# Kernel tuning notes

Measured on AMD Instinct MI355X. Metric: run time of the kernel, lower is better.

The kernel has to match this reference:

```python
import jax, jax.numpy as jnp
import numpy as np


def setup_inputs() -> dict:
    key = jax.random.key(0)
    k_x, k_rbf, k_nb, k_w1, k_w2 = jax.random.split(key, 5)
    N, NB, F_DIM, RBF_DIM = 20000, 32, 128, 64
    x = jax.random.normal(k_x, (N, F_DIM), dtype=jnp.float32)
    rbf = jax.random.uniform(k_rbf, (N, NB, RBF_DIM), dtype=jnp.float32)
    neighbors = jax.random.randint(k_nb, (N, NB), 0, N, dtype=jnp.int64)
    # filter network params (Linear(rbf_dim->f_dim), Softplus, Linear(f_dim->f_dim))
    w1 = jax.random.normal(k_w1, (RBF_DIM, F_DIM), dtype=jnp.float32) / np.sqrt(RBF_DIM)
    b1 = jnp.zeros((F_DIM,), dtype=jnp.float32)
    w2 = jax.random.normal(k_w2, (F_DIM, F_DIM), dtype=jnp.float32) / np.sqrt(F_DIM)
    b2 = jnp.zeros((F_DIM,), dtype=jnp.float32)
    return {"x": x, "rbf": rbf, "neighbors": neighbors,
            "w1": w1, "b1": b1, "w2": w2, "b2": b2}


def reference(x, rbf, neighbors, w1, b1, w2, b2):
    # filter network: Linear -> Softplus -> Linear, applied per (atom, neighbor)
    h = jax.nn.softplus(jnp.einsum('anr,rf->anf', rbf, w1) + b1)  # [N, NB, F]
    W = jnp.einsum('ang,gf->anf', h, w2) + b2                      # [N, NB, F]
    x_j = x[neighbors]                                             # gather [N, NB, F]
    return jnp.sum(x_j * W, axis=1)                                # [N, F]
```

## Files before the change

kernel.cpp:

```cpp
#include <hip/hip_runtime.h>
#include <math.h>


#define NATOMS 20000
#define NB     32
#define FD     128
#define RD     64
#define WAVES  8
#define NTILES 2500
#define HSTR   136

typedef short  short8  __attribute__((ext_vector_type(8)));
typedef float  floatx4 __attribute__((ext_vector_type(4)));
typedef float  floatx2 __attribute__((ext_vector_type(2)));

static __device__ __forceinline__ short f2bf(float f) {
  unsigned u = __builtin_bit_cast(unsigned, f);
  u = (u + 0x7FFFu + ((u >> 16) & 1u)) >> 16;
  return (short)u;
}

static __device__ __forceinline__ float softplus(float v) {
  return fmaxf(v, 0.0f) + __logf(1.0f + __expf(-fabsf(v)));
}

__global__ __launch_bounds__(512)
void cfconv_kernel(const float* __restrict__ x,
                   const float* __restrict__ rbf,
                   const int*   __restrict__ nbr,
                   const float* __restrict__ w1,
                   const float* __restrict__ b1,
                   const float* __restrict__ w2,
                   const float* __restrict__ b2,
                   float* __restrict__ out) {
  __shared__ __align__(16) short w1f[16][64][8];
  __shared__ __align__(16) short w2f[32][64][8];
  __shared__ __align__(16) short hbuf[WAVES * 32][HSTR];

  const int tid  = threadIdx.x;
  const int lane = tid & 63;
  const int wv   = tid >> 6;
  const int q    = lane >> 4;
  const int ln   = lane & 15;

  for (int i = tid; i < RD * FD; i += 512) {
    int k = i >> 7, n = i & 127, kk = k & 31;
    w1f[(k >> 5) * 8 + (n >> 4)][(kk >> 3) * 16 + (n & 15)][kk & 7] = f2bf(w1[i]);
  }
  for (int i = tid; i < FD * FD; i += 512) {
    int k = i >> 7, n = i & 127, kk = k & 31;
    w2f[(k >> 5) * 8 + (n >> 4)][(kk >> 3) * 16 + (n & 15)][kk & 7] = f2bf(w2[i]);
  }
  float b1v[8], b2v[8];
#pragma unroll
  for (int nt = 0; nt < 8; ++nt) {
    b1v[nt] = b1[nt * 16 + ln];
    b2v[nt] = b2[nt * 16 + ln];
  }
  __syncthreads();

  for (int tile = blockIdx.x; tile < NTILES; tile += gridDim.x) {
    const int atom = tile * WAVES + wv;
    const int prow = atom * NB;
    const int hrow = wv * 32;

    short8 afrag[2][2];
#pragma unroll
    for (int mt = 0; mt < 2; ++mt) {
      const float* src = rbf + (prow + mt * 16 + ln) * RD + q * 8;
#pragma unroll
      for (int kt = 0; kt < 2; ++kt) {
        floatx4 lo = *(const floatx4*)(src + kt * 32);
        floatx4 hi = *(const floatx4*)(src + kt * 32 + 4);
        short8 f;
        f[0] = f2bf(lo[0]); f[1] = f2bf(lo[1]); f[2] = f2bf(lo[2]); f[3] = f2bf(lo[3]);
        f[4] = f2bf(hi[0]); f[5] = f2bf(hi[1]); f[6] = f2bf(hi[2]); f[7] = f2bf(hi[3]);
        afrag[mt][kt] = f;
      }
    }

    floatx4 acc1[2][8];
#pragma unroll
    for (int mt = 0; mt < 2; ++mt)
#pragma unroll
      for (int nt = 0; nt < 8; ++nt)
        acc1[mt][nt] = floatx4{0.f, 0.f, 0.f, 0.f};
#pragma unroll
    for (int kt = 0; kt < 2; ++kt)
#pragma unroll
      for (int nt = 0; nt < 8; ++nt) {
        short8 bfrag = *(const short8*)&w1f[kt * 8 + nt][lane][0];
#pragma unroll
        for (int mt = 0; mt < 2; ++mt)
          acc1[mt][nt] = __builtin_amdgcn_mfma_f32_16x16x32_bf16(
              afrag[mt][kt], bfrag, acc1[mt][nt], 0, 0, 0);
      }

#pragma unroll
    for (int mt = 0; mt < 2; ++mt)
#pragma unroll
      for (int nt = 0; nt < 8; ++nt)
#pragma unroll
        for (int r = 0; r < 4; ++r)
          hbuf[hrow + mt * 16 + q * 4 + r][nt * 16 + ln] =
              f2bf(softplus(acc1[mt][nt][r] + b1v[nt]));

    short8 hfrag[2][4];
#pragma unroll
    for (int mt = 0; mt < 2; ++mt)
#pragma unroll
      for (int kt = 0; kt < 4; ++kt)
        hfrag[mt][kt] = *(const short8*)&hbuf[hrow + mt * 16 + ln][kt * 32 + q * 8];

    floatx4 acc2[2][8];
#pragma unroll
    for (int mt = 0; mt < 2; ++mt)
#pragma unroll
      for (int nt = 0; nt < 8; ++nt)
        acc2[mt][nt] = floatx4{0.f, 0.f, 0.f, 0.f};
#pragma unroll
    for (int kt = 0; kt < 4; ++kt)
#pragma unroll
      for (int nt = 0; nt < 8; ++nt) {
        short8 bfrag = *(const short8*)&w2f[kt * 8 + nt][lane][0];
#pragma unroll
        for (int mt = 0; mt < 2; ++mt)
          acc2[mt][nt] = __builtin_amdgcn_mfma_f32_16x16x32_bf16(
              hfrag[mt][kt], bfrag, acc2[mt][nt], 0, 0, 0);
      }

#pragma unroll
    for (int mt = 0; mt < 2; ++mt)
#pragma unroll
      for (int nt = 0; nt < 8; ++nt)
#pragma unroll
        for (int r = 0; r < 4; ++r)
          hbuf[hrow + mt * 16 + q * 4 + r][nt * 16 + ln] =
              f2bf(acc2[mt][nt][r] + b2v[nt]);

    const int* nbp = nbr + atom * NB;
    float o0 = 0.f, o1 = 0.f;
#pragma unroll 8
    for (int r = 0; r < NB; ++r) {
      int j = nbp[r];
      floatx2 xv = *(const floatx2*)(x + j * FD + lane * 2);
      unsigned pw = *(const unsigned*)&hbuf[hrow + r][lane * 2];
      o0 += xv[0] * __builtin_bit_cast(float, pw << 16);
      o1 += xv[1] * __builtin_bit_cast(float, pw & 0xFFFF0000u);
    }
    *(floatx2*)(out + atom * FD + lane * 2) = floatx2{o0, o1};
  }
}

extern "C" void kernel_launch(void* const* d_in, const int* in_sizes, int n_in,
                              void* d_out, int out_size, void* d_ws, size_t ws_size,
                              hipStream_t stream) {
  const float* x   = (const float*)d_in[0];
  const float* rbf = (const float*)d_in[1];
  const int*   nbr = (const int*)d_in[2];
  const float* w1  = (const float*)d_in[3];
  const float* b1  = (const float*)d_in[4];
  const float* w2  = (const float*)d_in[5];
  const float* b2  = (const float*)d_in[6];
  float* out = (float*)d_out;

  cfconv_kernel<<<dim3(256), dim3(512), 0, stream>>>(x, rbf, nbr, w1, b1, w2, b2, out);
}
```

Baseline: 310.1 us.

## Fuse second GEMM output directly into neighbor gather, shrink LDS band with XOR swizzle

```diff
diff --git a/kernel.cpp b/kernel.cpp
--- a/kernel.cpp
+++ b/kernel.cpp
@@ -1,30 +1,29 @@
 #include <hip/hip_runtime.h>
+#include <hip/hip_bf16.h>
 #include <math.h>
 
 
-#define NATOMS 20000
 #define NB     32
 #define FD     128
 #define RD     64
 #define WAVES  8
 #define NTILES 2500
-#define HSTR   136
 
 typedef short  short8  __attribute__((ext_vector_type(8)));
 typedef float  floatx4 __attribute__((ext_vector_type(4)));
-typedef float  floatx2 __attribute__((ext_vector_type(2)));
 
-static __device__ __forceinline__ short f2bf(float f) {
-  unsigned u = __builtin_bit_cast(unsigned, f);
-  u = (u + 0x7FFFu + ((u >> 16) & 1u)) >> 16;
-  return (short)u;
+static __device__ __forceinline__ unsigned pk2(float a, float b) {
+  __hip_bfloat162 h = __float22bfloat162_rn(float2{a, b});
+  unsigned u;
+  __builtin_memcpy(&u, &h, sizeof(u));
+  return u;
 }
 
 static __device__ __forceinline__ float softplus(float v) {
   return fmaxf(v, 0.0f) + __logf(1.0f + __expf(-fabsf(v)));
 }
 
-__global__ __launch_bounds__(512)
+__global__ __launch_bounds__(512, 4)
 void cfconv_kernel(const float* __restrict__ x,
                    const float* __restrict__ rbf,
                    const int*   __restrict__ nbr,
@@ -35,7 +34,7 @@
                    float* __restrict__ out) {
   __shared__ __align__(16) short w1f[16][64][8];
   __shared__ __align__(16) short w2f[32][64][8];
-  __shared__ __align__(16) short hbuf[WAVES * 32][HSTR];
+  __shared__ __align__(16) short hbuf[WAVES * 16][128];
 
   const int tid  = threadIdx.x;
   const int lane = tid & 63;
@@ -45,11 +44,11 @@
 
   for (int i = tid; i < RD * FD; i += 512) {
     int k = i >> 7, n = i & 127, kk = k & 31;
-    w1f[(k >> 5) * 8 + (n >> 4)][(kk >> 3) * 16 + (n & 15)][kk & 7] = f2bf(w1[i]);
+    w1f[(k >> 5) * 8 + (n >> 4)][(kk >> 3) * 16 + (n & 15)][kk & 7] = (short)pk2(w1[i], 0.f);
   }
   for (int i = tid; i < FD * FD; i += 512) {
     int k = i >> 7, n = i & 127, kk = k & 31;
-    w2f[(k >> 5) * 8 + (n >> 4)][(kk >> 3) * 16 + (n & 15)][kk & 7] = f2bf(w2[i]);
+    w2f[(k >> 5) * 8 + (n >> 4)][(kk >> 3) * 16 + (n & 15)][kk & 7] = (short)pk2(w2[i], 0.f);
   }
   float b1v[8], b2v[8];
 #pragma unroll
@@ -59,96 +58,107 @@
   }
   __syncthreads();
 
+  short (*band)[128] = &hbuf[wv * 16];
+
   for (int tile = blockIdx.x; tile < NTILES; tile += gridDim.x) {
     const int atom = tile * WAVES + wv;
     const int prow = atom * NB;
-    const int hrow = wv * 32;
 
-    short8 afrag[2][2];
+    floatx4 raw[2][2][2];
 #pragma unroll
     for (int mt = 0; mt < 2; ++mt) {
       const float* src = rbf + (prow + mt * 16 + ln) * RD + q * 8;
 #pragma unroll
       for (int kt = 0; kt < 2; ++kt) {
-        floatx4 lo = *(const floatx4*)(src + kt * 32);
-        floatx4 hi = *(const floatx4*)(src + kt * 32 + 4);
-        short8 f;
-        f[0] = f2bf(lo[0]); f[1] = f2bf(lo[1]); f[2] = f2bf(lo[2]); f[3] = f2bf(lo[3]);
-        f[4] = f2bf(hi[0]); f[5] = f2bf(hi[1]); f[6] = f2bf(hi[2]); f[7] = f2bf(hi[3]);
-        afrag[mt][kt] = f;
+        raw[mt][kt][0] = *(const floatx4*)(src + kt * 32);
+        raw[mt][kt][1] = *(const floatx4*)(src + kt * 32 + 4);
+      }
+    }
+    short8 afrag[2][2];
+#pragma unroll
+    for (int mt = 0; mt < 2; ++mt)
+#pragma unroll
+      for (int kt = 0; kt < 2; ++kt) {
+        union { short8 s8; unsigned u[4]; } f;
+        f.u[0] = pk2(raw[mt][kt][0][0], raw[mt][kt][0][1]);
+        f.u[1] = pk2(raw[mt][kt][0][2], raw[mt][kt][0][3]);
+        f.u[2] = pk2(raw[mt][kt][1][0], raw[mt][kt][1][1]);
+        f.u[3] = pk2(raw[mt][kt][1][2], raw[mt][kt][1][3]);
+        afrag[mt][kt] = f.s8;
+      }
+
+    const int* nbp = nbr + prow;
+    float psum[8];
+#pragma unroll
+    for (int nt = 0; nt < 8; ++nt) psum[nt] = 0.f;
+
+#pragma unroll
+    for (int mt = 0; mt < 2; ++mt) {
+      floatx4 acc1[8];
+#pragma unroll
+      for (int nt = 0; nt < 8; ++nt) acc1[nt] = floatx4{0.f, 0.f, 0.f, 0.f};
+#pragma unroll
+      for (int kt = 0; kt < 2; ++kt)
+#pragma unroll
+        for (int nt = 0; nt < 8; ++nt) {
+          short8 bfrag = *(const short8*)&w1f[kt * 8 + nt][lane][0];
+          acc1[nt] = __builtin_amdgcn_mfma_f32_16x16x32_bf16(
+              afrag[mt][kt], bfrag, acc1[nt], 0, 0, 0);
+        }
+
+#pragma unroll
+      for (int nt = 0; nt < 8; ++nt) {
+        const int c  = nt * 16 + ln;
+        const int cb = c >> 3, cl = c & 7;
+        float s0 = softplus(acc1[nt][0] + b1v[nt]);
+        float s1 = softplus(acc1[nt][1] + b1v[nt]);
+        float s2 = softplus(acc1[nt][2] + b1v[nt]);
+        float s3 = softplus(acc1[nt][3] + b1v[nt]);
+        unsigned u01 = pk2(s0, s1), u23 = pk2(s2, s3);
+        band[q * 4 + 0][(((cb ^ (q * 4 + 0)) & 15) << 3) | cl] = (short)u01;
+        band[q * 4 + 1][(((cb ^ (q * 4 + 1)) & 15) << 3) | cl] = (short)(u01 >> 16);
+        band[q * 4 + 2][(((cb ^ (q * 4 + 2)) & 15) << 3) | cl] = (short)u23;
+        band[q * 4 + 3][(((cb ^ (q * 4 + 3)) & 15) << 3) | cl] = (short)(u23 >> 16);
+      }
+
+      short8 hfrag[4];
+#pragma unroll
+      for (int kt = 0; kt < 4; ++kt) {
+        const int pb = ((kt * 4 + q) ^ ln) & 15;
+        hfrag[kt] = *(const short8*)&band[ln][pb << 3];
+      }
+
+      floatx4 acc2[8];
+#pragma unroll
+      for (int nt = 0; nt < 8; ++nt) acc2[nt] = floatx4{0.f, 0.f, 0.f, 0.f};
+#pragma unroll
+      for (int kt = 0; kt < 4; ++kt)
+#pragma unroll
+        for (int nt = 0; nt < 8; ++nt) {
+          short8 bfrag = *(const short8*)&w2f[kt * 8 + nt][lane][0];
+          acc2[nt] = __builtin_amdgcn_mfma_f32_16x16x32_bf16(
+              hfrag[kt], bfrag, acc2[nt], 0, 0, 0);
+        }
+
+#pragma unroll
+      for (int r = 0; r < 4; ++r) {
+        const int j = nbp[mt * 16 + q * 4 + r];
+        const float* xr = x + j * FD + ln;
+#pragma unroll
+        for (int nt = 0; nt < 8; ++nt)
+          psum[nt] = fmaf(xr[nt * 16], acc2[nt][r] + b2v[nt], psum[nt]);
       }
     }
 
-    floatx4 acc1[2][8];
 #pragma unroll
-    for (int mt = 0; mt < 2; ++mt)
-#pragma unroll
-      for (int nt = 0; nt < 8; ++nt)
-        acc1[mt][nt] = floatx4{0.f, 0.f, 0.f, 0.f};
-#pragma unroll
-    for (int kt = 0; kt < 2; ++kt)
-#pragma unroll
-      for (int nt = 0; nt < 8; ++nt) {
-        short8 bfrag = *(const short8*)&w1f[kt * 8 + nt][lane][0];
-#pragma unroll
-        for (int mt = 0; mt < 2; ++mt)
-          acc1[mt][nt] = __builtin_amdgcn_mfma_f32_16x16x32_bf16(
-              afrag[mt][kt], bfrag, acc1[mt][nt], 0, 0, 0);
-      }
-
-#pragma unroll
-    for (int mt = 0; mt < 2; ++mt)
-#pragma unroll
-      for (int nt = 0; nt < 8; ++nt)
-#pragma unroll
-        for (int r = 0; r < 4; ++r)
-          hbuf[hrow + mt * 16 + q * 4 + r][nt * 16 + ln] =
-              f2bf(softplus(acc1[mt][nt][r] + b1v[nt]));
-
-    short8 hfrag[2][4];
-#pragma unroll
-    for (int mt = 0; mt < 2; ++mt)
-#pragma unroll
-      for (int kt = 0; kt < 4; ++kt)
-        hfrag[mt][kt] = *(const short8*)&hbuf[hrow + mt * 16 + ln][kt * 32 + q * 8];
-
-    floatx4 acc2[2][8];
-#pragma unroll
-    for (int mt = 0; mt < 2; ++mt)
-#pragma unroll
-      for (int nt = 0; nt < 8; ++nt)
-        acc2[mt][nt] = floatx4{0.f, 0.f, 0.f, 0.f};
-#pragma unroll
-    for (int kt = 0; kt < 4; ++kt)
-#pragma unroll
-      for (int nt = 0; nt < 8; ++nt) {
-        short8 bfrag = *(const short8*)&w2f[kt * 8 + nt][lane][0];
-#pragma unroll
-        for (int mt = 0; mt < 2; ++mt)
-          acc2[mt][nt] = __builtin_amdgcn_mfma_f32_16x16x32_bf16(
-              hfrag[mt][kt], bfrag, acc2[mt][nt], 0, 0, 0);
-      }
-
-#pragma unroll
-    for (int mt = 0; mt < 2; ++mt)
-#pragma unroll
-      for (int nt = 0; nt < 8; ++nt)
-#pragma unroll
-        for (int r = 0; r < 4; ++r)
-          hbuf[hrow + mt * 16 + q * 4 + r][nt * 16 + ln] =
-              f2bf(acc2[mt][nt][r] + b2v[nt]);
-
-    const int* nbp = nbr + atom * NB;
-    float o0 = 0.f, o1 = 0.f;
-#pragma unroll 8
-    for (int r = 0; r < NB; ++r) {
-      int j = nbp[r];
-      floatx2 xv = *(const floatx2*)(x + j * FD + lane * 2);
-      unsigned pw = *(const unsigned*)&hbuf[hrow + r][lane * 2];
-      o0 += xv[0] * __builtin_bit_cast(float, pw << 16);
-      o1 += xv[1] * __builtin_bit_cast(float, pw & 0xFFFF0000u);
+    for (int nt = 0; nt < 8; ++nt) {
+      psum[nt] += __shfl_xor(psum[nt], 16);
+      psum[nt] += __shfl_xor(psum[nt], 32);
     }
-    *(floatx2*)(out + atom * FD + lane * 2) = floatx2{o0, o1};
+    float v0 = (q == 0) ? psum[0] : (q == 1) ? psum[2] : (q == 2) ? psum[4] : psum[6];
+    float v1 = (q == 0) ? psum[1] : (q == 1) ? psum[3] : (q == 2) ? psum[5] : psum[7];
+    out[atom * FD + q * 32 + ln]      = v0;
+    out[atom * FD + q * 32 + 16 + ln] = v1;
   }
 }
 
@@ -164,5 +174,5 @@
   const float* b2  = (const float*)d_in[6];
   float* out = (float*)d_out;
 
-  cfconv_kernel<<<dim3(256), dim3(512), 0, stream>>>(x, rbf, nbr, w1, b1, w2, b2, out);
+  cfconv_kernel<<<dim3(500), dim3(512), 0, stream>>>(x, rbf, nbr, w1, b1, w2, b2, out);
 }
```

New measurement: 627.7 us. +102.4%, slower.
